# Kernel optimization log

Hardware: AMD Instinct MI355X
Metric: run time of the kernel (lower is better)

## Reference

```python
import jax, jax.numpy as jnp
import numpy as np

EPS = 1e-5       # BatchNorm eps (eval mode, running_mean=0, running_var=1)
TV_F = 1e-5      # FLAGS.tv_reg_factor
CT_F = 1e-4      # FLAGS.constrast_reg_factor


def conv2d(x, w):
    return jax.lax.conv_general_dilated(x, w, (1, 1), 'SAME',
                                        dimension_numbers=('NCHW', 'OIHW', 'NCHW'))


def bn(x, p):
    # eval-mode BN with running_mean=0, running_var=1: x/sqrt(1+eps)*gamma + beta
    g, b = p[0], p[1]
    s = g / jnp.sqrt(1.0 + EPS)
    return x * s[None, :, None, None] + b[None, :, None, None]


def two_conv(x, w1, p1, w2, p2):
    x = jax.nn.relu(bn(conv2d(x, w1), p1))
    return jax.nn.relu(bn(conv2d(x, w2), p2))


def setup_inputs() -> dict:
    key = jax.random.key(0)
    ks = jax.random.split(key, 20)
    B, T, C, H = 8, 16, 2048, 7
    f = lambda k, sh, s=0.02: jax.random.normal(k, sh, jnp.float32) * s
    bnp = lambda k, c: jnp.stack([1.0 + f(k, (c,), 0.05), jnp.zeros((c,), jnp.float32)])
    return {
        'input_x': jax.random.normal(ks[0], (B, C, T, H, H), jnp.float32),
        'mask_w1': f(ks[1], (1024, 2048, 3, 3)), 'mask_bn1': bnp(ks[2], 1024),
        'mask_w2': f(ks[3], (512, 1024, 3, 3)), 'mask_bn2': bnp(ks[4], 512),
        'mask_w3': f(ks[5], (1, 512, 3, 3)),
        'h0_w1': f(ks[6], (1024, 2048, 3, 3)), 'h0_bn1': bnp(ks[7], 1024),
        'h0_w2': f(ks[8], (512, 1024, 3, 3)), 'h0_bn2': bnp(ks[9], 512),
        'c0_w1': f(ks[10], (1024, 2048, 3, 3)), 'c0_bn1': bnp(ks[11], 1024),
        'c0_w2': f(ks[12], (512, 1024, 3, 3)), 'c0_bn2': bnp(ks[13], 512),
        'att_fw': f(ks[14], (1, 2048)), 'att_hw': f(ks[15], (1, 512)),
        'lstm_w': f(ks[16], (4 * 512, 2048 + 512, 3, 3)),
        'lstm_b': jnp.zeros((4 * 512,), jnp.float32),
        'fc_w': f(ks[17], (3, 512)), 'fc_b': jnp.zeros((3,), jnp.float32),
    }


def reference(input_x, mask_w1, mask_bn1, mask_w2, mask_bn2, mask_w3,
              h0_w1, h0_bn1, h0_w2, h0_bn2, c0_w1, c0_bn1, c0_w2, c0_bn2,
              att_fw, att_hw, lstm_w, lstm_b, fc_w, fc_b):
    B, C, T, H, W = input_x.shape
    # dropout_2d is identity in eval mode
    xr = jnp.transpose(input_x, (0, 2, 1, 3, 4)).reshape(B * T, C, H, W)

    # mask conv: 2048 -> 1024 -> 512 -> 1, sigmoid
    m = jax.nn.relu(bn(conv2d(xr, mask_w1), mask_bn1))
    m = jax.nn.relu(bn(conv2d(m, mask_w2), mask_bn2))
    mask = jax.nn.sigmoid(conv2d(m, mask_w3)).reshape(B, T, 1, H, W)

    tv_loss = TV_F * (jnp.sum(jnp.abs(mask[..., 1:] - mask[..., :-1]))
                      + jnp.sum(jnp.abs(mask[..., 1:, :] - mask[..., :-1, :])))
    mA = (mask > 0.5).astype(jnp.float32)
    mB = (mask < 0.5).astype(jnp.float32)
    contrast_loss = (-(mask * mA).mean(0).sum() * CT_F * 0.5
                     + (mask * mB).mean(0).sum() * CT_F * 0.5)

    mx = mask * xr.reshape(B, T, C, H, W)          # (B,T,2048,7,7)
    mean_x = mx.mean(1)                            # (B,2048,7,7)
    h = two_conv(mean_x, h0_w1, h0_bn1, h0_w2, h0_bn2)   # (B,512,7,7)
    c = two_conv(mean_x, c0_w1, c0_bn1, c0_w2, c0_bn2)

    # per-frame feature attention logits (constant across steps)
    att_fea = (mx.mean((3, 4)) @ att_fw.T)[..., 0]       # (B,T)

    def step(carry, _):
        h, c = carry
        att_h = h.mean((2, 3)) @ att_hw.T                # (B,1)
        w = jax.nn.softmax(att_fea + att_h, axis=1)      # (B,T)
        xt = jnp.einsum('btchw,bt->bchw', mx, w)         # attention-weighted frame
        z = conv2d(jnp.concatenate([xt, h], axis=1), lstm_w) + lstm_b[None, :, None, None]
        i, f, o, g = jnp.split(z, 4, axis=1)
        c2 = jax.nn.sigmoid(f) * c + jax.nn.sigmoid(i) * jnp.tanh(g)
        h2 = jax.nn.sigmoid(o) * jnp.tanh(c2)
        return (h2, c2), (h2.mean((2, 3)), w)

    (_, _), (outs, ws) = jax.lax.scan(step, (h, c), None, length=T)
    final_output = outs.mean(0) @ fc_w.T + fc_b          # (B, output_size)
    return final_output, ws[-1], mask, tv_loss, contrast_loss


if __name__ == '__main__':
    out = reference(**setup_inputs())
    print(out[0].shape, out[1].shape, out[2].shape)
```

## Files before the change

### kernel.cpp

```cpp
#include <hip/hip_runtime.h>
#include <cstdint>

typedef unsigned short u16;
typedef __bf16 bf16x8 __attribute__((ext_vector_type(8)));
typedef float f32x4 __attribute__((ext_vector_type(4)));

#define BNRS 0.9999950000374997f

__device__ __forceinline__ u16 f2bf(float f) {
  unsigned u = __float_as_uint(f);
  u += 0x7fffu + ((u >> 16) & 1u);
  return (u16)(u >> 16);
}
__device__ __forceinline__ float bf2f(u16 h) {
  return __uint_as_float(((unsigned)h) << 16);
}

__device__ __forceinline__ void glds16(const u16* g, u16* l) {
  __builtin_amdgcn_global_load_lds(
      (const __attribute__((address_space(1))) void*)g,
      (__attribute__((address_space(3))) void*)l, 16, 0, 0);
}

#define OFF_XN     0ull
#define OFF_M1     42467328ull
#define OFF_M2     63700992ull
#define SZ_M2      10616832ull
#define OFF_MEANX  63700992ull
#define OFF_XTN    66355200ull
#define OFF_TH1    69009408ull
#define OFF_TC1    70336512ull
#define OFF_HN     71663616ull
#define OFF_CST    72327168ull
#define OFF_ZXACC  74317824ull
#define OFF_ATH1   77529088ull
#define OFF_ATC1   79134720ull
#define OFF_ATH2   80740352ull
#define OFF_ATC2   81543168ull
#define OFF_FEA    82345984ull
#define OFF_W      82346496ull
#define OFF_OUTS   82347008ull
#define Z0_END     82378752ull
#define OFF_WA     82378752ull
#define OFF_WB     120127488ull
#define OFF_MX     129564672ull
#define OFF_LSTMW  82378752ull
#define OFF_ZPART  176750592ull
#define ARENA_END  202440704ull

#define CF_BN    1
#define CF_RELU  2
#define CF_ATOM  4
#define CF_OUTF  8
#define CF_OUTB 16
#define CF_ZOFF 32

__global__ __launch_bounds__(256)
void k_conv(const u16* __restrict__ Xin, const u16* __restrict__ Wt,
            float* __restrict__ outF, u16* __restrict__ outB,
            float* __restrict__ atomF,
            const float* __restrict__ gamma, const float* __restrict__ beta,
            int M, int Cin, int log2Cin, int ldb, int Cout, int kChunk, int flags)
{
  __shared__ u16 As[128*32];
  __shared__ u16 Bs[128*32];
  const int tid = threadIdx.x;
  const int m0 = blockIdx.x*128, n0 = blockIdx.y*128;
  const int row0 = tid >> 2, c8 = (tid & 3) * 8;

  long long Abase[2], Bbase[2];
  #pragma unroll
  for (int r = 0; r < 2; ++r) {
    int m = m0 + row0 + r*64; if (m > M-1) m = M-1;
    int img = m / 49, p = m % 49, y = p / 7, xx = p % 7;
    Abase[r] = (long long)(img*81 + y*9 + xx) * Cin + c8;
    Bbase[r] = (long long)(n0 + row0 + r*64) * ldb + c8;
  }
  const long long tapStride = (long long)Cout * ldb;
  const int lane = tid & 63, wave = tid >> 6;
  const int l16 = lane & 15, quad = lane >> 4;
  const int wm = wave & 1, wn = wave >> 1;
  const u16* Afr = As + (wm*64 + l16)*32 + quad*8;
  const u16* Bfr = Bs + (wn*64 + l16)*32 + quad*8;
  u16* ldsA0 = As + wave*512;
  u16* ldsA1 = As + 2048 + wave*512;
  u16* ldsB0 = Bs + wave*512;
  u16* ldsB1 = Bs + 2048 + wave*512;

  f32x4 acc[4][4];
  #pragma unroll
  for (int i=0;i<4;i++)
    #pragma unroll
    for (int j=0;j<4;j++)
      #pragma unroll
      for (int r=0;r<4;r++) acc[i][j][r] = 0.f;

  const int kStart = blockIdx.z * kChunk, kEnd = kStart + kChunk;
  for (int kk = kStart; kk < kEnd; kk += 32) {
    int tap = kk >> log2Cin;
    int kc  = kk & (Cin - 1);
    int ty  = tap / 3;
    int tapAdd = (ty*6 + tap) << log2Cin;
    const u16* ga0 = Xin + Abase[0] + tapAdd + kc;
    const u16* ga1 = Xin + Abase[1] + tapAdd + kc;
    const u16* wp  = Wt + (long long)tap * tapStride + kc;
    const u16* gb0 = wp + Bbase[0];
    const u16* gb1 = wp + Bbase[1];
    __syncthreads();
    glds16(ga0, ldsA0);
    glds16(ga1, ldsA1);
    glds16(gb0, ldsB0);
    glds16(gb1, ldsB1);
    __syncthreads();
    bf16x8 av[4], bv[4];
    #pragma unroll
    for (int i=0;i<4;i++) av[i] = *(const bf16x8*)(Afr + i*16*32);
    #pragma unroll
    for (int j=0;j<4;j++) bv[j] = *(const bf16x8*)(Bfr + j*16*32);
    #pragma unroll
    for (int i=0;i<4;i++)
      #pragma unroll
      for (int j=0;j<4;j++)
        acc[i][j] = __builtin_amdgcn_mfma_f32_16x16x32_bf16(av[i], bv[j], acc[i][j], 0, 0, 0);
  }

  float* outFz = outF;
  if (flags & CF_ZOFF) outFz = outF + (long long)blockIdx.z * M * Cout;
  #pragma unroll
  for (int i=0;i<4;i++) {
    #pragma unroll
    for (int r=0;r<4;r++) {
      int m = m0 + wm*64 + i*16 + quad*4 + r;
      if (m >= M) continue;
      int img = m / 49, p = m % 49;
      int pp = (p/7 + 1)*9 + (p%7) + 1;
      #pragma unroll
      for (int j=0;j<4;j++) {
        int n = n0 + wn*64 + j*16 + l16;
        float v = acc[i][j][r];
        if (flags & CF_BN)   v = v * (gamma[n]*BNRS) + beta[n];
        if (flags & CF_RELU) v = fmaxf(v, 0.f);
        if (flags & CF_ATOM) atomicAdd(atomF + (long long)m*Cout + n, v);
        if (flags & CF_OUTF) outFz[(long long)m*Cout + n] = v;
        if (flags & CF_OUTB) outB[((long long)img*81 + pp)*Cout + n] = f2bf(v);
      }
    }
  }
}

__global__ void k_wtrans(const float* __restrict__ W, u16* __restrict__ Wt, int total) {
  int idx = blockIdx.x*256 + threadIdx.x;
  if (idx >= total) return;
  const float* src = W + (long long)idx*9;
  #pragma unroll
  for (int tap=0; tap<9; ++tap)
    Wt[(long long)tap*total + idx] = f2bf(src[tap]);
}

__global__ void k_transpose(const float* __restrict__ x, u16* __restrict__ Xn) {
  int idx = blockIdx.x*256 + threadIdx.x;
  int p = idx % 49; int r = idx / 49; int c8 = (r & 255)*8; int b = r >> 8;
  if (b >= 8) return;
  int pp = (p/7 + 1)*9 + (p%7) + 1;
  for (int t=0; t<16; ++t) {
    u16 o[8];
    #pragma unroll
    for (int j=0;j<8;j++)
      o[j] = f2bf(x[((long long)(b*2048 + c8 + j)*16 + t)*49 + p]);
    *(uint4*)&Xn[((long long)(b*16+t)*81 + pp)*2048 + c8] = *(uint4*)o;
  }
}

__global__ void k_mask3(const u16* __restrict__ M2b, const float* __restrict__ w3,
                        float* __restrict__ maskOut) {
  int img = blockIdx.x / 49, p = blockIdx.x % 49;
  int y = p/7, xx = p%7;
  int lane = threadIdx.x;
  float s = 0.f;
  for (int k = lane; k < 4608; k += 64) {
    int tap = k >> 9, c = k & 511;
    int ty = tap/3, tx = tap - ty*3;
    int pp = (y+ty)*9 + xx + tx;
    s += bf2f(M2b[((long long)img*81 + pp)*512 + c]) * w3[c*9 + tap];
  }
  #pragma unroll
  for (int off=32; off>0; off>>=1) s += __shfl_down(s, off, 64);
  if (lane == 0) maskOut[blockIdx.x] = 1.f/(1.f + expf(-s));
}

__global__ void k_losses(const float* __restrict__ mk, float* __restrict__ dout) {
  __shared__ float s1[256], s2[256];
  int tid = threadIdx.x;
  float tv = 0.f, ct = 0.f;
  for (int i = tid; i < 128*7*6; i += 256) {
    int img = i / 42, r = i % 42, y = r / 6, xx = r % 6;
    int base = img*49 + y*7 + xx;
    tv += fabsf(mk[base+1] - mk[base]);
  }
  for (int i = tid; i < 128*6*7; i += 256) {
    int img = i / 42, r = i % 42, y = r / 7, xx = r % 7;
    int base = img*49 + y*7 + xx;
    tv += fabsf(mk[base+7] - mk[base]);
  }
  for (int i = tid; i < 6272; i += 256) {
    float v = mk[i];
    ct += (v < 0.5f ? v : 0.f) - (v > 0.5f ? v : 0.f);
  }
  s1[tid] = tv; s2[tid] = ct; __syncthreads();
  for (int off=128; off>0; off>>=1) {
    if (tid < off) { s1[tid]+=s1[tid+off]; s2[tid]+=s2[tid+off]; }
    __syncthreads();
  }
  if (tid==0) { dout[6424] = 1e-5f * s1[0]; dout[6425] = (1e-4f*0.5f/8.f) * s2[0]; }
}

__global__ void k_mx(const float* __restrict__ x, const float* __restrict__ mk,
                     u16* __restrict__ mxn, u16* __restrict__ meanx) {
  int idx = blockIdx.x*256 + threadIdx.x;
  int p = idx % 49; int r = idx / 49; int c8 = (r & 255)*8; int b = r >> 8;
  if (b >= 8) return;
  int pp = (p/7+1)*9 + (p%7) + 1;
  float macc[8] = {0,0,0,0,0,0,0,0};
  for (int t=0;t<16;++t) {
    float mval = mk[(b*16+t)*49 + p];
    u16 o[8];
    #pragma unroll
    for (int j=0;j<8;j++) {
      float v = x[((long long)(b*2048 + c8 + j)*16 + t)*49 + p] * mval;
      o[j] = f2bf(v); macc[j] += v;
    }
    *(uint4*)&mxn[((long long)(b*16+t)*81 + pp)*2048 + c8] = *(uint4*)o;
  }
  u16 o2[8];
  #pragma unroll
  for (int j=0;j<8;j++) o2[j] = f2bf(macc[j] * (1.f/16.f));
  *(uint4*)&meanx[((long long)b*81 + pp)*2048 + c8] = *(uint4*)o2;
}

__global__ void k_att(const u16* __restrict__ mxn, const float* __restrict__ fw,
                      float* __restrict__ fea) {
  __shared__ float red[256];
  int img = blockIdx.x, tid = threadIdx.x;
  const u16* base = mxn + (long long)img*81*2048;
  float s = 0.f;
  for (int k = tid; k < 49*2048; k += 256) {
    int p = k >> 11, c = k & 2047;
    int pp = (p/7+1)*9 + (p%7) + 1;
    s += bf2f(base[(long long)pp*2048 + c]) * fw[c];
  }
  red[tid] = s; __syncthreads();
  for (int off=128; off>0; off>>=1) { if (tid<off) red[tid]+=red[tid+off]; __syncthreads(); }
  if (tid==0) fea[img] = red[0] * (1.f/49.f);
}

__global__ void k_softmax(const float* __restrict__ fea, float* __restrict__ w,
                          float* __restrict__ doutW) {
  int b = threadIdx.x;
  if (b >= 8) return;
  float mx = -1e30f;
  for (int t=0;t<16;t++) mx = fmaxf(mx, fea[b*16+t]);
  float e[16], s = 0.f;
  for (int t=0;t<16;t++) { e[t] = expf(fea[b*16+t]-mx); s += e[t]; }
  float inv = 1.f/s;
  for (int t=0;t<16;t++) { float v = e[t]*inv; w[b*16+t] = v; doutW[b*16+t] = v; }
}

__global__ void k_xt(const u16* __restrict__ mxn, const float* __restrict__ w,
                     u16* __restrict__ xtn) {
  int idx = blockIdx.x*256 + threadIdx.x;
  int c8 = (idx & 255)*8; int r = idx >> 8; int p = r % 49; int b = r / 49;
  if (b >= 8) return;
  int pp = (p/7+1)*9 + (p%7)+1;
  float a[8] = {0,0,0,0,0,0,0,0};
  for (int t=0;t<16;t++) {
    float wt = w[b*16+t];
    uint4 raw = *(const uint4*)&mxn[((long long)(b*16+t)*81 + pp)*2048 + c8];
    const u16* h = (const u16*)&raw;
    #pragma unroll
    for (int j=0;j<8;j++) a[j] += wt * bf2f(h[j]);
  }
  u16 o[8];
  #pragma unroll
  for (int j=0;j<8;j++) o[j] = f2bf(a[j]);
  *(uint4*)&xtn[((long long)b*81+pp)*2048 + c8] = *(uint4*)o;
}

__global__ void k_finalize(const float* __restrict__ acc, const float* __restrict__ bn,
                           u16* __restrict__ outB, float* __restrict__ outF, int C) {
  int idx = blockIdx.x*256 + threadIdx.x;
  int total = 8*81*C;
  if (idx >= total) return;
  int c = idx % C; int r = idx / C; int pp = r % 81; int img = r / 81;
  int py = pp/9, px = pp%9;
  bool inter = (py>=1 && py<=7 && px>=1 && px<=7);
  float v = 0.f;
  int m = img*49 + (py-1)*7 + (px-1);
  if (inter) {
    v = acc[(long long)m*C + c];
    v = v*(bn[c]*BNRS) + bn[C+c];
    v = fmaxf(v, 0.f);
  }
  if (outB) outB[idx] = f2bf(v);
  if (outF && inter) outF[(long long)m*C + c] = v;
}

__global__ void k_gate(const float* __restrict__ zx, const float* __restrict__ zp,
                       const float* __restrict__ lb, float* __restrict__ cst,
                       u16* __restrict__ hn, float* __restrict__ outs) {
  int idx = blockIdx.x*256 + threadIdx.x;
  if (idx >= 392*512) return;
  int c = idx & 511; int m = idx >> 9;
  int b = m / 49, p = m % 49;
  int pp = (p/7+1)*9 + (p%7)+1;
  const float* zr = zx + (long long)m*2048;
  float zi = zr[c]        + lb[c];
  float zf = zr[c+512]    + lb[c+512];
  float zo = zr[c+1024]   + lb[c+1024];
  float zg = zr[c+1536]   + lb[c+1536];
  #pragma unroll
  for (int s=0;s<8;s++) {
    const float* q = zp + ((long long)s*392 + m)*2048;
    zi += q[c]; zf += q[c+512]; zo += q[c+1024]; zg += q[c+1536];
  }
  float si = 1.f/(1.f+expf(-zi));
  float sf = 1.f/(1.f+expf(-zf));
  float so = 1.f/(1.f+expf(-zo));
  float cn = sf*cst[idx] + si*tanhf(zg);
  float h  = so*tanhf(cn);
  cst[idx] = cn;
  hn[((long long)b*81 + pp)*512 + c] = f2bf(h);
  atomicAdd(outs + b*512 + c, h*(1.f/784.f));
}

__global__ void k_fc(const float* __restrict__ outs, const float* __restrict__ fcw,
                     const float* __restrict__ fcb, float* __restrict__ dout) {
  int t = threadIdx.x;
  if (t >= 24) return;
  int b = t / 3, j = t % 3;
  float s = fcb[j];
  for (int c=0;c<512;c++) s += outs[b*512+c]*fcw[j*512+c];
  dout[b*3+j] = s;
}

extern "C" void kernel_launch(void* const* d_in, const int* in_sizes, int n_in,
                              void* d_out, int out_size, void* d_ws, size_t ws_size,
                              hipStream_t stream) {
  (void)in_sizes; (void)n_in; (void)out_size;
  const float* x        = (const float*)d_in[0];
  const float* mask_w1  = (const float*)d_in[1];
  const float* mask_bn1 = (const float*)d_in[2];
  const float* mask_w2  = (const float*)d_in[3];
  const float* mask_bn2 = (const float*)d_in[4];
  const float* mask_w3  = (const float*)d_in[5];
  const float* h0_w1    = (const float*)d_in[6];
  const float* h0_bn1   = (const float*)d_in[7];
  const float* h0_w2    = (const float*)d_in[8];
  const float* h0_bn2   = (const float*)d_in[9];
  const float* c0_w1    = (const float*)d_in[10];
  const float* c0_bn1   = (const float*)d_in[11];
  const float* c0_w2    = (const float*)d_in[12];
  const float* c0_bn2   = (const float*)d_in[13];
  const float* att_fw   = (const float*)d_in[14];
  const float* lstm_w   = (const float*)d_in[16];
  const float* lstm_b   = (const float*)d_in[17];
  const float* fc_w     = (const float*)d_in[18];
  const float* fc_b     = (const float*)d_in[19];
  float* dout = (float*)d_out;
  char* ws = (char*)d_ws;
  if (ws_size < ARENA_END) return;

  u16* XN    = (u16*)(ws + OFF_XN);
  u16* M1b   = (u16*)(ws + OFF_M1);
  u16* M2b   = (u16*)(ws + OFF_M2);
  u16* MEANX = (u16*)(ws + OFF_MEANX);
  u16* XTN   = (u16*)(ws + OFF_XTN);
  u16* TH1   = (u16*)(ws + OFF_TH1);
  u16* TC1   = (u16*)(ws + OFF_TC1);
  u16* HN    = (u16*)(ws + OFF_HN);
  float* CST   = (float*)(ws + OFF_CST);
  float* ZXACC = (float*)(ws + OFF_ZXACC);
  float* ATH1  = (float*)(ws + OFF_ATH1);
  float* ATC1  = (float*)(ws + OFF_ATC1);
  float* ATH2  = (float*)(ws + OFF_ATH2);
  float* ATC2  = (float*)(ws + OFF_ATC2);
  float* FEA   = (float*)(ws + OFF_FEA);
  float* Wbuf  = (float*)(ws + OFF_W);
  float* OUTS  = (float*)(ws + OFF_OUTS);
  u16* WA    = (u16*)(ws + OFF_WA);
  u16* WB    = (u16*)(ws + OFF_WB);
  u16* MX    = (u16*)(ws + OFF_MX);
  u16* LSTMW = (u16*)(ws + OFF_LSTMW);
  float* ZPART = (float*)(ws + OFF_ZPART);

  hipMemsetAsync(ws, 0, (size_t)Z0_END, stream);

  k_wtrans<<<8192, 256, 0, stream>>>(mask_w1, WA, 1024*2048);
  k_wtrans<<<2048, 256, 0, stream>>>(mask_w2, WB, 512*1024);
  k_transpose<<<392, 256, 0, stream>>>(x, XN);
  k_conv<<<dim3(49,8,1),256,0,stream>>>(XN, WA, nullptr, M1b, nullptr,
      mask_bn1, mask_bn1+1024, 6272, 2048, 11, 2048, 1024, 18432, CF_BN|CF_RELU|CF_OUTB);
  k_conv<<<dim3(49,4,1),256,0,stream>>>(M1b, WB, nullptr, M2b, nullptr,
      mask_bn2, mask_bn2+512, 6272, 1024, 10, 1024, 512, 9216, CF_BN|CF_RELU|CF_OUTB);
  k_mask3<<<6272, 64, 0, stream>>>(M2b, mask_w3, dout+152);
  k_losses<<<1, 256, 0, stream>>>(dout+152, dout);

  hipMemsetAsync(ws + OFF_M2, 0, (size_t)SZ_M2, stream);
  k_mx<<<392, 256, 0, stream>>>(x, dout+152, MX, MEANX);
  k_att<<<128, 256, 0, stream>>>(MX, att_fw, FEA);
  k_softmax<<<1, 64, 0, stream>>>(FEA, Wbuf, dout+24);
  k_xt<<<392, 256, 0, stream>>>(MX, Wbuf, XTN);

  k_wtrans<<<8192, 256, 0, stream>>>(h0_w1, WA, 1024*2048);
  k_wtrans<<<2048, 256, 0, stream>>>(h0_w2, WB, 512*1024);
  k_conv<<<dim3(4,8,8),256,0,stream>>>(MEANX, WA, nullptr, nullptr, ATH1,
      nullptr, nullptr, 392, 2048, 11, 2048, 1024, 2304, CF_ATOM);
  k_finalize<<<2592, 256, 0, stream>>>(ATH1, h0_bn1, TH1, nullptr, 1024);
  k_conv<<<dim3(4,4,8),256,0,stream>>>(TH1, WB, nullptr, nullptr, ATH2,
      nullptr, nullptr, 392, 1024, 10, 1024, 512, 1152, CF_ATOM);
  k_finalize<<<1296, 256, 0, stream>>>(ATH2, h0_bn2, HN, nullptr, 512);

  k_wtrans<<<8192, 256, 0, stream>>>(c0_w1, WA, 1024*2048);
  k_wtrans<<<2048, 256, 0, stream>>>(c0_w2, WB, 512*1024);
  k_conv<<<dim3(4,8,8),256,0,stream>>>(MEANX, WA, nullptr, nullptr, ATC1,
      nullptr, nullptr, 392, 2048, 11, 2048, 1024, 2304, CF_ATOM);
  k_finalize<<<2592, 256, 0, stream>>>(ATC1, c0_bn1, TC1, nullptr, 1024);
  k_conv<<<dim3(4,4,8),256,0,stream>>>(TC1, WB, nullptr, nullptr, ATC2,
      nullptr, nullptr, 392, 1024, 10, 1024, 512, 1152, CF_ATOM);
  k_finalize<<<1296, 256, 0, stream>>>(ATC2, c0_bn2, nullptr, CST, 512);

  k_wtrans<<<20480, 256, 0, stream>>>(lstm_w, LSTMW, 2048*2560);
  k_conv<<<dim3(4,16,8),256,0,stream>>>(XTN, LSTMW, nullptr, nullptr, ZXACC,
      nullptr, nullptr, 392, 2048, 11, 2560, 2048, 2304, CF_ATOM);
  for (int step = 0; step < 16; ++step) {
    k_conv<<<dim3(4,16,8),256,0,stream>>>(HN, LSTMW+2048, ZPART, nullptr, nullptr,
        nullptr, nullptr, 392, 512, 9, 2560, 2048, 576, CF_OUTF|CF_ZOFF);
    k_gate<<<784, 256, 0, stream>>>(ZXACC, ZPART, lstm_b, CST, HN, OUTS);
  }
  k_fc<<<1, 64, 0, stream>>>(OUTS, fc_w, fc_b, dout);
}
```

Before: 2.479 ms.

## Swizzle LDS layout, split-K mask convs with atomics, deepen split-K elsewhere

Adds an XOR swizzle to the LDS tile layout for the A/B fragments so the MFMA fragment reads avoid bank conflicts. The two big mask convolutions (6272 rows) now use 4-way split-K with atomic float accumulation plus a separate finalize kernel for BN+ReLU and bf16 conversion, instead of a single pass that fused BN. The small h0/c0/LSTM-input convs double their split-K depth to 16 to fill more CUs. The price is extra atomic traffic, a memset of about 38 MB of accumulators, and an extra finalize pass for each mask layer.

```diff
diff --git a/kernel.cpp b/kernel.cpp
--- a/kernel.cpp
+++ b/kernel.cpp
@@ -44,6 +44,9 @@
 #define OFF_WA     82378752ull
 #define OFF_WB     120127488ull
 #define OFF_MX     129564672ull
+#define OFF_M1ACC  129564672ull
+#define OFF_M2ACC  155254784ull
+#define SZ_MACC    38535168ull
 #define OFF_LSTMW  82378752ull
 #define OFF_ZPART  176750592ull
 #define ARENA_END  202440704ull
@@ -66,7 +69,8 @@
   __shared__ u16 Bs[128*32];
   const int tid = threadIdx.x;
   const int m0 = blockIdx.x*128, n0 = blockIdx.y*128;
-  const int row0 = tid >> 2, c8 = (tid & 3) * 8;
+  const int row0 = tid >> 2;
+  const int c8 = (((tid & 3) ^ (row0 & 3) ^ ((row0 >> 2) & 3))) * 8;
 
   long long Abase[2], Bbase[2];
   #pragma unroll
@@ -80,8 +84,9 @@
   const int lane = tid & 63, wave = tid >> 6;
   const int l16 = lane & 15, quad = lane >> 4;
   const int wm = wave & 1, wn = wave >> 1;
-  const u16* Afr = As + (wm*64 + l16)*32 + quad*8;
-  const u16* Bfr = Bs + (wn*64 + l16)*32 + quad*8;
+  const int fsl = (quad ^ (l16 & 3) ^ ((l16 >> 2) & 3)) * 8;
+  const u16* Afr = As + (wm*64 + l16)*32 + fsl;
+  const u16* Bfr = Bs + (wn*64 + l16)*32 + fsl;
   u16* ldsA0 = As + wave*512;
   u16* ldsA1 = As + 2048 + wave*512;
   u16* ldsB0 = Bs + wave*512;
@@ -286,9 +291,10 @@
 }
 
 __global__ void k_finalize(const float* __restrict__ acc, const float* __restrict__ bn,
-                           u16* __restrict__ outB, float* __restrict__ outF, int C) {
-  int idx = blockIdx.x*256 + threadIdx.x;
-  int total = 8*81*C;
+                           u16* __restrict__ outB, float* __restrict__ outF,
+                           int C, int nImg) {
+  int idx = blockIdx.x*256 + threadIdx.x;
+  int total = nImg*81*C;
   if (idx >= total) return;
   int c = idx % C; int r = idx / C; int pp = r % 81; int img = r / 81;
   int py = pp/9, px = pp%9;
@@ -391,16 +397,21 @@
   u16* MX    = (u16*)(ws + OFF_MX);
   u16* LSTMW = (u16*)(ws + OFF_LSTMW);
   float* ZPART = (float*)(ws + OFF_ZPART);
+  float* M1ACC = (float*)(ws + OFF_M1ACC);
+  float* M2ACC = (float*)(ws + OFF_M2ACC);
 
   hipMemsetAsync(ws, 0, (size_t)Z0_END, stream);
+  hipMemsetAsync(ws + OFF_M1ACC, 0, (size_t)SZ_MACC, stream);
 
   k_wtrans<<<8192, 256, 0, stream>>>(mask_w1, WA, 1024*2048);
   k_wtrans<<<2048, 256, 0, stream>>>(mask_w2, WB, 512*1024);
   k_transpose<<<392, 256, 0, stream>>>(x, XN);
-  k_conv<<<dim3(49,8,1),256,0,stream>>>(XN, WA, nullptr, M1b, nullptr,
-      mask_bn1, mask_bn1+1024, 6272, 2048, 11, 2048, 1024, 18432, CF_BN|CF_RELU|CF_OUTB);
-  k_conv<<<dim3(49,4,1),256,0,stream>>>(M1b, WB, nullptr, M2b, nullptr,
-      mask_bn2, mask_bn2+512, 6272, 1024, 10, 1024, 512, 9216, CF_BN|CF_RELU|CF_OUTB);
+  k_conv<<<dim3(49,8,4),256,0,stream>>>(XN, WA, nullptr, nullptr, M1ACC,
+      nullptr, nullptr, 6272, 2048, 11, 2048, 1024, 4608, CF_ATOM);
+  k_finalize<<<41472, 256, 0, stream>>>(M1ACC, mask_bn1, M1b, nullptr, 1024, 128);
+  k_conv<<<dim3(49,4,4),256,0,stream>>>(M1b, WB, nullptr, nullptr, M2ACC,
+      nullptr, nullptr, 6272, 1024, 10, 1024, 512, 2304, CF_ATOM);
+  k_finalize<<<20736, 256, 0, stream>>>(M2ACC, mask_bn2, M2b, nullptr, 512, 128);
   k_mask3<<<6272, 64, 0, stream>>>(M2b, mask_w3, dout+152);
   k_losses<<<1, 256, 0, stream>>>(dout+152, dout);
 
@@ -412,25 +423,25 @@
 
   k_wtrans<<<8192, 256, 0, stream>>>(h0_w1, WA, 1024*2048);
   k_wtrans<<<2048, 256, 0, stream>>>(h0_w2, WB, 512*1024);
-  k_conv<<<dim3(4,8,8),256,0,stream>>>(MEANX, WA, nullptr, nullptr, ATH1,
-      nullptr, nullptr, 392, 2048, 11, 2048, 1024, 2304, CF_ATOM);
-  k_finalize<<<2592, 256, 0, stream>>>(ATH1, h0_bn1, TH1, nullptr, 1024);
-  k_conv<<<dim3(4,4,8),256,0,stream>>>(TH1, WB, nullptr, nullptr, ATH2,
-      nullptr, nullptr, 392, 1024, 10, 1024, 512, 1152, CF_ATOM);
-  k_finalize<<<1296, 256, 0, stream>>>(ATH2, h0_bn2, HN, nullptr, 512);
+  k_conv<<<dim3(4,8,16),256,0,stream>>>(MEANX, WA, nullptr, nullptr, ATH1,
+      nullptr, nullptr, 392, 2048, 11, 2048, 1024, 1152, CF_ATOM);
+  k_finalize<<<2592, 256, 0, stream>>>(ATH1, h0_bn1, TH1, nullptr, 1024, 8);
+  k_conv<<<dim3(4,4,16),256,0,stream>>>(TH1, WB, nullptr, nullptr, ATH2,
+      nullptr, nullptr, 392, 1024, 10, 1024, 512, 576, CF_ATOM);
+  k_finalize<<<1296, 256, 0, stream>>>(ATH2, h0_bn2, HN, nullptr, 512, 8);
 
   k_wtrans<<<8192, 256, 0, stream>>>(c0_w1, WA, 1024*2048);
   k_wtrans<<<2048, 256, 0, stream>>>(c0_w2, WB, 512*1024);
-  k_conv<<<dim3(4,8,8),256,0,stream>>>(MEANX, WA, nullptr, nullptr, ATC1,
-      nullptr, nullptr, 392, 2048, 11, 2048, 1024, 2304, CF_ATOM);
-  k_finalize<<<2592, 256, 0, stream>>>(ATC1, c0_bn1, TC1, nullptr, 1024);
-  k_conv<<<dim3(4,4,8),256,0,stream>>>(TC1, WB, nullptr, nullptr, ATC2,
-      nullptr, nullptr, 392, 1024, 10, 1024, 512, 1152, CF_ATOM);
-  k_finalize<<<1296, 256, 0, stream>>>(ATC2, c0_bn2, nullptr, CST, 512);
+  k_conv<<<dim3(4,8,16),256,0,stream>>>(MEANX, WA, nullptr, nullptr, ATC1,
+      nullptr, nullptr, 392, 2048, 11, 2048, 1024, 1152, CF_ATOM);
+  k_finalize<<<2592, 256, 0, stream>>>(ATC1, c0_bn1, TC1, nullptr, 1024, 8);
+  k_conv<<<dim3(4,4,16),256,0,stream>>>(TC1, WB, nullptr, nullptr, ATC2,
+      nullptr, nullptr, 392, 1024, 10, 1024, 512, 576, CF_ATOM);
+  k_finalize<<<1296, 256, 0, stream>>>(ATC2, c0_bn2, nullptr, CST, 512, 8);
 
   k_wtrans<<<20480, 256, 0, stream>>>(lstm_w, LSTMW, 2048*2560);
-  k_conv<<<dim3(4,16,8),256,0,stream>>>(XTN, LSTMW, nullptr, nullptr, ZXACC,
-      nullptr, nullptr, 392, 2048, 11, 2560, 2048, 2304, CF_ATOM);
+  k_conv<<<dim3(4,16,16),256,0,stream>>>(XTN, LSTMW, nullptr, nullptr, ZXACC,
+      nullptr, nullptr, 392, 2048, 11, 2560, 2048, 1152, CF_ATOM);
   for (int step = 0; step < 16; ++step) {
     k_conv<<<dim3(4,16,8),256,0,stream>>>(HN, LSTMW+2048, ZPART, nullptr, nullptr,
         nullptr, nullptr, 392, 512, 9, 2560, 2048, 576, CF_OUTF|CF_ZOFF);
```

Result: faster. 2.297 ms (-7.3%).
